# Kernel optimization log

Hardware: AMD Instinct MI355X
Metric: run time of the kernel (lower is better)

Reference implementation:

```python
import jax, jax.numpy as jnp
import numpy as np

B, N, M = 8192, 4096, 256


def setup_inputs() -> dict:
    key = jax.random.key(0)
    k_x, k_keep, k_w1, k_b1, k_w2, k_b2 = jax.random.split(key, 6)
    x = jax.random.normal(k_x, (B, N), dtype=jnp.float32)
    keep = jax.random.uniform(k_keep, (B, N)) < 0.5
    x = jnp.where(keep, x, 0.0)
    # Linear params, PyTorch-style fan-in scaling
    W1 = jax.random.normal(k_w1, (N, M), dtype=jnp.float32) / np.sqrt(N)
    b1 = jax.random.normal(k_b1, (M,), dtype=jnp.float32) * 0.01
    W2 = jax.random.normal(k_w2, (M, N), dtype=jnp.float32) / np.sqrt(M)
    b2 = jax.random.normal(k_b2, (N,), dtype=jnp.float32) * 0.01
    return {"x": x, "W1": W1, "b1": b1, "W2": W2, "b2": b2}


def reference(x, W1, b1, W2, b2):
    # f2(relu(f1(x)))
    f = jax.nn.relu(x @ W1 + b1) @ W2 + b2  # [B, N]
    mask = x != 0
    # per-row sum over masked positions (vectorized version of the Python loop)
    s = jnp.sum(jnp.where(mask, f, 0.0), axis=1, keepdims=True)  # [B, 1]
    # rows with empty mask stay all-zero; guard divide-by-zero for those rows
    s_safe = jnp.where(s == 0.0, 1.0, s)
    y = jnp.where(mask, f / s_safe, 0.0)
    return y
```

## Files before the change

kernel.cpp:

```cpp
#include <hip/hip_runtime.h>

typedef _Float16 f16;
typedef _Float16 f16x8 __attribute__((ext_vector_type(8)));
typedef float f32x4 __attribute__((ext_vector_type(4)));

#define MFMA16(a,b,c) __builtin_amdgcn_mfma_f32_16x16x32_f16((a),(b),(c),0,0,0)

__device__ __forceinline__ void gload16(const void* g, void* l) {
  __builtin_amdgcn_global_load_lds(
      (const __attribute__((address_space(1))) void*)g,
      (__attribute__((address_space(3))) void*)l, 16, 0, 0);
}

__device__ __forceinline__ int swz(int r, int c) {
  return r * 32 + ((c ^ ((r >> 1) & 3)) << 3);
}

__device__ __forceinline__ void split8n(const f32x4 v0, const f32x4 v1,
                                        f16x8& hv, f16x8& lv) {
#pragma unroll
  for (int j = 0; j < 4; ++j) {
    f16 h0 = (f16)v0[j]; hv[j] = h0; lv[j] = (f16)(v0[j] - (float)h0);
    f16 h1 = (f16)v1[j]; hv[j + 4] = h1; lv[j + 4] = (f16)(v1[j] - (float)h1);
  }
}

__global__ __launch_bounds__(256) void k_prep(const float* __restrict__ in,
                                              f16* __restrict__ oh, f16* __restrict__ ol,
                                              int R, int C, int trShift) {
  __shared__ float t[64][65];
  int c0 = blockIdx.x * 64, r0 = blockIdx.y * 64;
  int tid = threadIdx.x;
#pragma unroll
  for (int i = 0; i < 16; ++i) {
    int idx = tid + i * 256;
    int r = idx >> 6, c = idx & 63;
    t[r][c] = in[(size_t)(r0 + r) * C + (c0 + c)];
  }
  __syncthreads();
  int ktiles = R >> 5;
  int TRm1 = (1 << trShift) - 1;
#pragma unroll
  for (int w = 0; w < 2; ++w) {
    int idx = tid + w * 256;
    int nn = idx >> 3, cc8 = idx & 7;
    f32x4 v0, v1;
#pragma unroll
    for (int j = 0; j < 4; ++j) v0[j] = t[cc8 * 8 + j][nn];
#pragma unroll
    for (int j = 0; j < 4; ++j) v1[j] = t[cc8 * 8 + 4 + j][nn];
    f16x8 hv, lv;
    split8n(v0, v1, hv, lv);
    int gn = c0 + nn, gk = r0 + cc8 * 8;
    size_t tileIdx = (size_t)(gn >> trShift) * ktiles + (gk >> 5);
    size_t off = (tileIdx << (trShift + 5)) + ((size_t)(gn & TRm1) << 5) +
                 (((cc8 & 3) ^ ((gn >> 1) & 3)) << 3);
    *(f16x8*)&oh[off] = hv;
    *(f16x8*)&ol[off] = lv;
  }
}

__global__ __launch_bounds__(256, 3) void k_g1(
    const float* __restrict__ X, const f16* __restrict__ Bht,
    const f16* __restrict__ Blt, unsigned char* __restrict__ mb,
    float* __restrict__ partials) {
  __shared__ f16 smB[3][8192];
  int bx = blockIdx.x, nb = blockIdx.y, kc = blockIdx.z;
  int tid = threadIdx.x;
  int wv = tid >> 6, ln = tid & 63, lr = ln & 15, lg = ln >> 4;
  const int NS = 32;
  int m0 = bx * 128, kb0 = kc * 1024;
  size_t bt0 = ((size_t)nb * 128 + (size_t)kc * 32) * 4096;
  bool domask = (nb == 0);

  const float* xb = X + (size_t)(m0 + wv * 32 + lr) * 4096 + kb0 + lg * 8;
  const size_t XF = (size_t)16 * 4096;

  f32x4 areg[4];
  f16x8 ah[2], al[2];
  f32x4 acc[2][8] = {};

  auto issueA = [&](int s) {
#pragma unroll
    for (int fi = 0; fi < 2; ++fi) {
      const float* p = xb + (size_t)fi * XF + s * 32;
      areg[fi * 2] = *(const f32x4*)p;
      areg[fi * 2 + 1] = *(const f32x4*)(p + 4);
    }
  };
  auto stageB = [&](int s, int buf) {
    const f16* bh = Bht + bt0 + (size_t)s * 4096;
    const f16* bl = Blt + bt0 + (size_t)s * 4096;
#pragma unroll
    for (int i = 0; i < 2; ++i)
      gload16(bh + ((i * 4 + wv) * 512 + ln * 8), &smB[buf][(i * 4 + wv) * 512]);
#pragma unroll
    for (int i = 0; i < 2; ++i)
      gload16(bl + ((i * 4 + wv) * 512 + ln * 8),
              &smB[buf][4096 + (i * 4 + wv) * 512]);
  };
  auto splitA = [&](int s) {
#pragma unroll
    for (int fi = 0; fi < 2; ++fi)
      split8n(areg[fi * 2], areg[fi * 2 + 1], ah[fi], al[fi]);
    if (domask) {
#pragma unroll
      for (int fi = 0; fi < 2; ++fi) {
        unsigned m = 0;
#pragma unroll
        for (int j = 0; j < 4; ++j) {
          if (areg[fi * 2][j] != 0.f) m |= 1u << j;
          if (areg[fi * 2 + 1][j] != 0.f) m |= 1u << (4 + j);
        }
        int row = m0 + wv * 32 + fi * 16 + lr;
        int gk = kb0 + s * 32 + lg * 8;
        mb[(size_t)row * 512 + (gk >> 3)] = (unsigned char)m;
      }
    }
  };

  issueA(0);
  stageB(0, 0);
  stageB(1, 1);
  asm volatile("s_waitcnt vmcnt(4)" ::: "memory");
  __builtin_amdgcn_sched_barrier(0);
  splitA(0);
  __builtin_amdgcn_s_barrier();

  int cb = 0;
  for (int s = 0; s < NS; ++s) {
    bool moreA = (s + 1) < NS;
    bool moreB = (s + 2) < NS;
    if (moreA) issueA(s + 1);
    if (moreB) {
      int pb = cb + 2; if (pb >= 3) pb -= 3;
      stageB(s + 2, pb);
    }
#pragma unroll
    for (int g = 0; g < 2; ++g) {
      f16x8 fbh[4], fbl[4];
#pragma unroll
      for (int j = 0; j < 4; ++j) {
        int c = (g * 4 + j) * 16 + lr;
        fbh[j] = *(const f16x8*)&smB[cb][swz(c, lg)];
        fbl[j] = *(const f16x8*)&smB[cb][4096 + swz(c, lg)];
      }
#pragma unroll
      for (int fi = 0; fi < 2; ++fi)
#pragma unroll
        for (int j = 0; j < 4; ++j) {
          acc[fi][g * 4 + j] = MFMA16(ah[fi], fbh[j], acc[fi][g * 4 + j]);
          acc[fi][g * 4 + j] = MFMA16(ah[fi], fbl[j], acc[fi][g * 4 + j]);
          acc[fi][g * 4 + j] = MFMA16(al[fi], fbh[j], acc[fi][g * 4 + j]);
        }
    }
    if (moreA) {
      if (moreB)
        asm volatile("s_waitcnt vmcnt(4)" ::: "memory");
      else
        asm volatile("s_waitcnt vmcnt(0)" ::: "memory");
      __builtin_amdgcn_sched_barrier(0);
      splitA(s + 1);
      __builtin_amdgcn_s_barrier();
    }
    cb = cb + 1; if (cb >= 3) cb -= 3;
  }

  float* pout = partials + (size_t)kc * 8192 * 256;
#pragma unroll
  for (int fi = 0; fi < 2; ++fi)
#pragma unroll
    for (int fj = 0; fj < 8; ++fj)
#pragma unroll
      for (int q = 0; q < 4; ++q) {
        int row = m0 + wv * 32 + fi * 16 + lg * 4 + q;
        int col = nb * 128 + fj * 16 + lr;
        pout[(size_t)row * 256 + col] = acc[fi][fj][q];
      }
}

__global__ __launch_bounds__(256) void k_hsplit(const float* __restrict__ p,
                                                const float* __restrict__ b1,
                                                f16* __restrict__ Hh,
                                                f16* __restrict__ Hl) {
  int g = blockIdx.x * 256 + threadIdx.x;
  int r = g >> 5, c = g & 31;
  const size_t CH = (size_t)8192 * 256;
  const float* p0 = p + (size_t)r * 256 + c * 8;
  f32x4 s0 = *(const f32x4*)p0, s1 = *(const f32x4*)(p0 + 4);
#pragma unroll
  for (int q = 1; q < 4; ++q) {
    f32x4 d0 = *(const f32x4*)(p0 + q * CH), d1 = *(const f32x4*)(p0 + q * CH + 4);
#pragma unroll
    for (int j = 0; j < 4; ++j) { s0[j] += d0[j]; s1[j] += d1[j]; }
  }
  f32x4 bb0 = *(const f32x4*)(b1 + c * 8), bb1 = *(const f32x4*)(b1 + c * 8 + 4);
  f32x4 v0, v1;
#pragma unroll
  for (int j = 0; j < 4; ++j) {
    float v = s0[j] + bb0[j];
    v0[j] = v > 0.f ? v : 0.f;
    float w = s1[j] + bb1[j];
    v1[j] = w > 0.f ? w : 0.f;
  }
  f16x8 hv, lv;
  split8n(v0, v1, hv, lv);
  size_t tileIdx = (size_t)(r >> 8) * 8 + (c >> 2);
  size_t off = tileIdx * 8192 + ((size_t)(r & 255) << 5) +
               (((c & 3) ^ ((r >> 1) & 3)) << 3);
  *(f16x8*)&Hh[off] = hv;
  *(f16x8*)&Hl[off] = lv;
}

__global__ __launch_bounds__(512, 1) void k_gemm2c(
    const f16* __restrict__ At_h, const f16* __restrict__ At_l,
    const f16* __restrict__ Bt_h, const f16* __restrict__ Bt_l,
    const float* __restrict__ b2, const unsigned* __restrict__ maskw,
    f16* __restrict__ fout, float* __restrict__ partials) {
  __shared__ f16 smA[2][2][8192];
  __shared__ f16 smB[2][2][8192];
  __shared__ unsigned mlds[256][8];
  __shared__ float rsum[256][2];
  int bx = blockIdx.x, by = blockIdx.y;
  int m0 = bx * 256, n0 = by * 256;
  int tid = threadIdx.x;
  int wid = tid >> 6, ln = tid & 63, lr = ln & 15, lg = ln >> 4;
  int wr = wid >> 1, wc = wid & 1;
#pragma unroll
  for (int i = 0; i < 4; ++i) {
    int idx = tid + i * 512;
    mlds[idx >> 3][idx & 7] =
        maskw[(size_t)(m0 + (idx >> 3)) * 128 + by * 8 + (idx & 7)];
  }
  size_t at0 = (size_t)bx * 8 * 8192;
  size_t bt0 = (size_t)by * 8 * 8192;

  auto stage = [&](int s, int buf) {
#pragma unroll
    for (int i = 0; i < 2; ++i) {
      size_t o = (size_t)(i * 8 + wid) * 512 + (size_t)ln * 8;
      gload16(At_h + at0 + (size_t)s * 8192 + o, &smA[buf][0][(i * 8 + wid) * 512]);
      gload16(At_l + at0 + (size_t)s * 8192 + o, &smA[buf][1][(i * 8 + wid) * 512]);
      gload16(Bt_h + bt0 + (size_t)s * 8192 + o, &smB[buf][0][(i * 8 + wid) * 512]);
      gload16(Bt_l + bt0 + (size_t)s * 8192 + o, &smB[buf][1][(i * 8 + wid) * 512]);
    }
  };

  f32x4 acc[4][8] = {};
  stage(0, 0);
  __syncthreads();
  int cur = 0;
  for (int s = 0; s < 8; ++s) {
    if (s + 1 < 8) stage(s + 1, cur ^ 1);
    f16x8 fah[4], fal[4];
#pragma unroll
    for (int f = 0; f < 4; ++f) {
      int r = wr * 64 + f * 16 + lr;
      fah[f] = *(const f16x8*)&smA[cur][0][swz(r, lg)];
      fal[f] = *(const f16x8*)&smA[cur][1][swz(r, lg)];
    }
#pragma unroll
    for (int g = 0; g < 2; ++g) {
      f16x8 fbh[4], fbl[4];
#pragma unroll
      for (int j = 0; j < 4; ++j) {
        int c = wc * 128 + (g * 4 + j) * 16 + lr;
        fbh[j] = *(const f16x8*)&smB[cur][0][swz(c, lg)];
        fbl[j] = *(const f16x8*)&smB[cur][1][swz(c, lg)];
      }
#pragma unroll
      for (int fi = 0; fi < 4; ++fi)
#pragma unroll
        for (int j = 0; j < 4; ++j) {
          acc[fi][g * 4 + j] = MFMA16(fah[fi], fbh[j], acc[fi][g * 4 + j]);
          acc[fi][g * 4 + j] = MFMA16(fah[fi], fbl[j], acc[fi][g * 4 + j]);
          acc[fi][g * 4 + j] = MFMA16(fal[fi], fbh[j], acc[fi][g * 4 + j]);
        }
    }
    __syncthreads();
    cur ^= 1;
  }

  float rp[4][4] = {};
#pragma unroll
  for (int fi = 0; fi < 4; ++fi)
#pragma unroll
    for (int fj = 0; fj < 8; ++fj)
#pragma unroll
      for (int q = 0; q < 4; ++q) {
        int row = wr * 64 + fi * 16 + lg * 4 + q;
        int col = wc * 128 + fj * 16 + lr;
        float v = acc[fi][fj][q] + b2[n0 + col];
        unsigned wd = mlds[row][col >> 5];
        float mv = ((wd >> (col & 31)) & 1u) ? v : 0.f;
        fout[(size_t)(m0 + row) * 4096 + (n0 + col)] = (f16)mv;
        rp[fi][q] += mv;
      }
#pragma unroll
  for (int fi = 0; fi < 4; ++fi)
#pragma unroll
    for (int q = 0; q < 4; ++q) {
      float sv = rp[fi][q];
      sv += __shfl_xor(sv, 1);
      sv += __shfl_xor(sv, 2);
      sv += __shfl_xor(sv, 4);
      sv += __shfl_xor(sv, 8);
      if (lr == 0) rsum[wr * 64 + fi * 16 + lg * 4 + q][wc] = sv;
    }
  __syncthreads();
  if (tid < 256)
    partials[(size_t)(m0 + tid) * 16 + by] = rsum[tid][0] + rsum[tid][1];
}

__global__ __launch_bounds__(256) void k_rowinv(const float* __restrict__ partials,
                                                float* __restrict__ inv) {
  int r = blockIdx.x * 256 + threadIdx.x;
  if (r < 8192) {
    float s = 0.f;
#pragma unroll 4
    for (int i = 0; i < 16; ++i) s += partials[(size_t)r * 16 + i];
    float ss = (s == 0.f) ? 1.f : s;
    inv[r] = 1.f / ss;
  }
}

__global__ __launch_bounds__(256) void k_scale16(const f16* __restrict__ f,
                                                 const float* __restrict__ inv,
                                                 float* __restrict__ out) {
  int v = blockIdx.x * 256 + threadIdx.x;
  float iv = inv[v >> 9];
  f16x8 d = *(const f16x8*)(f + (size_t)v * 8);
  f32x4 o0, o1;
#pragma unroll
  for (int j = 0; j < 4; ++j) {
    o0[j] = (float)d[j] * iv;
    o1[j] = (float)d[4 + j] * iv;
  }
  *(f32x4*)(out + (size_t)v * 8) = o0;
  *(f32x4*)(out + (size_t)v * 8 + 4) = o1;
}

extern "C" void kernel_launch(void* const* d_in, const int* in_sizes, int n_in,
                              void* d_out, int out_size, void* d_ws, size_t ws_size,
                              hipStream_t stream) {
  const float* x  = (const float*)d_in[0];
  const float* W1 = (const float*)d_in[1];
  const float* b1 = (const float*)d_in[2];
  const float* W2 = (const float*)d_in[3];
  const float* b2 = (const float*)d_in[4];
  float* out = (float*)d_out;
  char* ws = (char*)d_ws;

  const size_t MB = (size_t)1 << 20;
  f16* W1t_h = (f16*)(ws + 0 * MB);
  f16* W1t_l = (f16*)(ws + 2 * MB);
  f16* W2t_h = (f16*)(ws + 4 * MB);
  f16* W2t_l = (f16*)(ws + 6 * MB);
  f16* Hh    = (f16*)(ws + 8 * MB);
  f16* Hl    = (f16*)(ws + 12 * MB);
  unsigned char* mb = (unsigned char*)(ws + 16 * MB);
  float* part1 = (float*)(ws + 20 * MB);
  float* part2 = (float*)(ws + 52 * MB);
  float* inv_s = (float*)(ws + 53 * MB);
  f16* fbuf    = (f16*)(ws + 54 * MB);

  k_prep<<<dim3(4, 64), 256, 0, stream>>>(W1, W1t_h, W1t_l, 4096, 256, 7);
  k_prep<<<dim3(64, 4), 256, 0, stream>>>(W2, W2t_h, W2t_l, 256, 4096, 8);
  k_g1<<<dim3(64, 2, 4), 256, 0, stream>>>(x, W1t_h, W1t_l, mb, part1);
  k_hsplit<<<1024, 256, 0, stream>>>(part1, b1, Hh, Hl);
  k_gemm2c<<<dim3(32, 16), 512, 0, stream>>>(Hh, Hl, W2t_h, W2t_l, b2,
                                             (const unsigned*)mb, fbuf, part2);
  k_rowinv<<<32, 256, 0, stream>>>(part2, inv_s);
  k_scale16<<<16384, 256, 0, stream>>>(fbuf, inv_s, out);
}
```

Before: 188.1 us.

## Double K-step per stage in GEMM1 and fuse row-inverse into scale kernel

```diff
diff --git a/kernel.cpp b/kernel.cpp
--- a/kernel.cpp
+++ b/kernel.cpp
@@ -60,15 +60,15 @@
   }
 }
 
-__global__ __launch_bounds__(256, 3) void k_g1(
+__global__ __launch_bounds__(256, 2) void k_g1(
     const float* __restrict__ X, const f16* __restrict__ Bht,
     const f16* __restrict__ Blt, unsigned char* __restrict__ mb,
     float* __restrict__ partials) {
-  __shared__ f16 smB[3][8192];
+  __shared__ f16 smB[2][16384];
   int bx = blockIdx.x, nb = blockIdx.y, kc = blockIdx.z;
   int tid = threadIdx.x;
   int wv = tid >> 6, ln = tid & 63, lr = ln & 15, lg = ln >> 4;
-  const int NS = 32;
+  const int NS = 16;
   int m0 = bx * 128, kb0 = kc * 1024;
   size_t bt0 = ((size_t)nb * 128 + (size_t)kc * 32) * 4096;
   bool domask = (nb == 0);
@@ -76,94 +76,99 @@
   const float* xb = X + (size_t)(m0 + wv * 32 + lr) * 4096 + kb0 + lg * 8;
   const size_t XF = (size_t)16 * 4096;
 
-  f32x4 areg[4];
-  f16x8 ah[2], al[2];
+  f32x4 areg[8];
+  f16x8 ah[2][2], al[2][2];
   f32x4 acc[2][8] = {};
 
   auto issueA = [&](int s) {
 #pragma unroll
-    for (int fi = 0; fi < 2; ++fi) {
-      const float* p = xb + (size_t)fi * XF + s * 32;
-      areg[fi * 2] = *(const f32x4*)p;
-      areg[fi * 2 + 1] = *(const f32x4*)(p + 4);
-    }
+    for (int fi = 0; fi < 2; ++fi)
+#pragma unroll
+      for (int kk = 0; kk < 2; ++kk) {
+        const float* p = xb + (size_t)fi * XF + s * 64 + kk * 32;
+        areg[fi * 4 + kk * 2] = *(const f32x4*)p;
+        areg[fi * 4 + kk * 2 + 1] = *(const f32x4*)(p + 4);
+      }
   };
   auto stageB = [&](int s, int buf) {
-    const f16* bh = Bht + bt0 + (size_t)s * 4096;
-    const f16* bl = Blt + bt0 + (size_t)s * 4096;
-#pragma unroll
-    for (int i = 0; i < 2; ++i)
+    const f16* bh = Bht + bt0 + (size_t)s * 8192;
+    const f16* bl = Blt + bt0 + (size_t)s * 8192;
+#pragma unroll
+    for (int i = 0; i < 4; ++i)
       gload16(bh + ((i * 4 + wv) * 512 + ln * 8), &smB[buf][(i * 4 + wv) * 512]);
 #pragma unroll
-    for (int i = 0; i < 2; ++i)
+    for (int i = 0; i < 4; ++i)
       gload16(bl + ((i * 4 + wv) * 512 + ln * 8),
-              &smB[buf][4096 + (i * 4 + wv) * 512]);
+              &smB[buf][8192 + (i * 4 + wv) * 512]);
   };
   auto splitA = [&](int s) {
 #pragma unroll
     for (int fi = 0; fi < 2; ++fi)
-      split8n(areg[fi * 2], areg[fi * 2 + 1], ah[fi], al[fi]);
+#pragma unroll
+      for (int kk = 0; kk < 2; ++kk)
+        split8n(areg[fi * 4 + kk * 2], areg[fi * 4 + kk * 2 + 1],
+                ah[fi][kk], al[fi][kk]);
     if (domask) {
 #pragma unroll
-      for (int fi = 0; fi < 2; ++fi) {
-        unsigned m = 0;
-#pragma unroll
-        for (int j = 0; j < 4; ++j) {
-          if (areg[fi * 2][j] != 0.f) m |= 1u << j;
-          if (areg[fi * 2 + 1][j] != 0.f) m |= 1u << (4 + j);
+      for (int fi = 0; fi < 2; ++fi)
+#pragma unroll
+        for (int kk = 0; kk < 2; ++kk) {
+          const f32x4& a0 = areg[fi * 4 + kk * 2];
+          const f32x4& a1 = areg[fi * 4 + kk * 2 + 1];
+          unsigned m = 0;
+#pragma unroll
+          for (int j = 0; j < 4; ++j) {
+            if (a0[j] != 0.f) m |= 1u << j;
+            if (a1[j] != 0.f) m |= 1u << (4 + j);
+          }
+          int row = m0 + wv * 32 + fi * 16 + lr;
+          int gk = kb0 + s * 64 + kk * 32 + lg * 8;
+          mb[(size_t)row * 512 + (gk >> 3)] = (unsigned char)m;
         }
-        int row = m0 + wv * 32 + fi * 16 + lr;
-        int gk = kb0 + s * 32 + lg * 8;
-        mb[(size_t)row * 512 + (gk >> 3)] = (unsigned char)m;
-      }
     }
   };
 
   issueA(0);
   stageB(0, 0);
-  stageB(1, 1);
-  asm volatile("s_waitcnt vmcnt(4)" ::: "memory");
+  asm volatile("s_waitcnt vmcnt(0)" ::: "memory");
   __builtin_amdgcn_sched_barrier(0);
   splitA(0);
   __builtin_amdgcn_s_barrier();
 
-  int cb = 0;
+  int cur = 0;
   for (int s = 0; s < NS; ++s) {
-    bool moreA = (s + 1) < NS;
-    bool moreB = (s + 2) < NS;
-    if (moreA) issueA(s + 1);
-    if (moreB) {
-      int pb = cb + 2; if (pb >= 3) pb -= 3;
-      stageB(s + 2, pb);
-    }
-#pragma unroll
-    for (int g = 0; g < 2; ++g) {
-      f16x8 fbh[4], fbl[4];
-#pragma unroll
-      for (int j = 0; j < 4; ++j) {
-        int c = (g * 4 + j) * 16 + lr;
-        fbh[j] = *(const f16x8*)&smB[cb][swz(c, lg)];
-        fbl[j] = *(const f16x8*)&smB[cb][4096 + swz(c, lg)];
-      }
-#pragma unroll
-      for (int fi = 0; fi < 2; ++fi)
+    bool more = (s + 1) < NS;
+    if (more) {
+      issueA(s + 1);
+      stageB(s + 1, cur ^ 1);
+    }
+#pragma unroll
+    for (int kk = 0; kk < 2; ++kk)
+#pragma unroll
+      for (int g = 0; g < 2; ++g) {
+        f16x8 fbh[4], fbl[4];
 #pragma unroll
         for (int j = 0; j < 4; ++j) {
-          acc[fi][g * 4 + j] = MFMA16(ah[fi], fbh[j], acc[fi][g * 4 + j]);
-          acc[fi][g * 4 + j] = MFMA16(ah[fi], fbl[j], acc[fi][g * 4 + j]);
-          acc[fi][g * 4 + j] = MFMA16(al[fi], fbh[j], acc[fi][g * 4 + j]);
+          int c = (g * 4 + j) * 16 + lr;
+          fbh[j] = *(const f16x8*)&smB[cur][kk * 4096 + swz(c, lg)];
+          fbl[j] = *(const f16x8*)&smB[cur][8192 + kk * 4096 + swz(c, lg)];
         }
-    }
-    if (moreA) {
-      if (moreB)
-        asm volatile("s_waitcnt vmcnt(4)" ::: "memory");
-      else
-        asm volatile("s_waitcnt vmcnt(0)" ::: "memory");
+#pragma unroll
+        for (int fi = 0; fi < 2; ++fi)
+#pragma unroll
+          for (int j = 0; j < 4; ++j) {
+            acc[fi][g * 4 + j] = MFMA16(ah[fi][kk], fbh[j], acc[fi][g * 4 + j]);
+            acc[fi][g * 4 + j] = MFMA16(ah[fi][kk], fbl[j], acc[fi][g * 4 + j]);
+            acc[fi][g * 4 + j] = MFMA16(al[fi][kk], fbh[j], acc[fi][g * 4 + j]);
+          }
+      }
+    if (more) {
+      asm volatile("s_waitcnt vmcnt(0)" ::: "memory");
       __builtin_amdgcn_sched_barrier(0);
       splitA(s + 1);
       __builtin_amdgcn_s_barrier();
     }
-    cb = cb + 1; if (cb >= 3) cb -= 3;
+    cur ^= 1;
   }
 
   float* pout = partials + (size_t)kc * 8192 * 256;
@@ -312,32 +317,30 @@
     partials[(size_t)(m0 + tid) * 16 + by] = rsum[tid][0] + rsum[tid][1];
 }
 
-__global__ __launch_bounds__(256) void k_rowinv(const float* __restrict__ partials,
-                                                float* __restrict__ inv) {
-  int r = blockIdx.x * 256 + threadIdx.x;
-  if (r < 8192) {
+__global__ __launch_bounds__(256) void k_scale16(const f16* __restrict__ f,
+                                                 const float* __restrict__ partials,
+                                                 float* __restrict__ out) {
+  __shared__ float sinv;
+  int tid = threadIdx.x;
+  int row = blockIdx.x >> 1;
+  if (tid == 0) {
     float s = 0.f;
-#pragma unroll 4
-    for (int i = 0; i < 16; ++i) s += partials[(size_t)r * 16 + i];
-    float ss = (s == 0.f) ? 1.f : s;
-    inv[r] = 1.f / ss;
-  }
-}
-
-__global__ __launch_bounds__(256) void k_scale16(const f16* __restrict__ f,
-                                                 const float* __restrict__ inv,
-                                                 float* __restrict__ out) {
-  int v = blockIdx.x * 256 + threadIdx.x;
-  float iv = inv[v >> 9];
-  f16x8 d = *(const f16x8*)(f + (size_t)v * 8);
+#pragma unroll
+    for (int i = 0; i < 16; ++i) s += partials[(size_t)row * 16 + i];
+    sinv = 1.f / ((s == 0.f) ? 1.f : s);
+  }
+  __syncthreads();
+  float iv = sinv;
+  size_t v = (size_t)blockIdx.x * 256 + tid;
+  f16x8 d = *(const f16x8*)(f + v * 8);
   f32x4 o0, o1;
 #pragma unroll
   for (int j = 0; j < 4; ++j) {
     o0[j] = (float)d[j] * iv;
     o1[j] = (float)d[4 + j] * iv;
   }
-  *(f32x4*)(out + (size_t)v * 8) = o0;
-  *(f32x4*)(out + (size_t)v * 8 + 4) = o1;
+  *(f32x4*)(out + v * 8) = o0;
+  *(f32x4*)(out + v * 8 + 4) = o1;
 }
 
 extern "C" void kernel_launch(void* const* d_in, const int* in_sizes, int n_in,
@@ -361,7 +364,6 @@
   unsigned char* mb = (unsigned char*)(ws + 16 * MB);
   float* part1 = (float*)(ws + 20 * MB);
   float* part2 = (float*)(ws + 52 * MB);
-  float* inv_s = (float*)(ws + 53 * MB);
   f16* fbuf    = (f16*)(ws + 54 * MB);
 
   k_prep<<<dim3(4, 64), 256, 0, stream>>>(W1, W1t_h, W1t_l, 4096, 256, 7);
@@ -370,6 +372,5 @@
   k_hsplit<<<1024, 256, 0, stream>>>(part1, b1, Hh, Hl);
   k_gemm2c<<<dim3(32, 16), 512, 0, stream>>>(Hh, Hl, W2t_h, W2t_l, b2,
                                              (const unsigned*)mb, fbuf, part2);
-  k_rowinv<<<32, 256, 0, stream>>>(part2, inv_s);
-  k_scale16<<<16384, 256, 0, stream>>>(fbuf, inv_s, out);
-}
+  k_scale16<<<16384, 256, 0, stream>>>(fbuf, part2, out);
+}
```

Measured after the change: 187.4 us. Within noise of the previous version (-0.4%).
